# Kernel tuning notes

Hardware: AMD Instinct MI355X
Metric: run time of the kernel (lower is better)

Reference implementation:

```python
import jax, jax.numpy as jnp
import numpy as np

B, N, DIM_IN, DIM_OUT, EMBED, CHEB_K = 32, 2000, 64, 64, 16, 3


def setup_inputs() -> dict:
    key = jax.random.key(0)
    ks = jax.random.split(key, 6)
    return {
        "x": jax.random.normal(ks[0], (B, N, DIM_IN), dtype=jnp.float32),
        "node_embeddings": jax.random.normal(ks[1], (N, EMBED), dtype=jnp.float32),
        "nodevec1": jax.random.normal(ks[2], (N, EMBED), dtype=jnp.float32),
        "nodevec2": jax.random.normal(ks[3], (EMBED, N), dtype=jnp.float32),
        "weights_pool": jax.random.normal(ks[4], (EMBED, CHEB_K, DIM_IN, DIM_OUT), dtype=jnp.float32) * 0.1,
        "bias_pool": jax.random.normal(ks[5], (EMBED, DIM_OUT), dtype=jnp.float32) * 0.1,
    }


def reference(x, node_embeddings, nodevec1, nodevec2, weights_pool, bias_pool):
    n = node_embeddings.shape[0]
    # adaptive adjacency: softmax(relu(nodevec1 @ nodevec2)) over rows' neighbors
    s = jax.nn.softmax(jax.nn.relu(nodevec1 @ nodevec2), axis=1)  # [N, N]
    # Chebyshev polynomial stack: T0 = I, T1 = S, Tk = 2 S Tk-1 - Tk-2
    support_set = [jnp.eye(n, dtype=x.dtype), s]
    for _ in range(2, CHEB_K):
        support_set.append(2.0 * s @ support_set[-1] - support_set[-2])
    supports = jnp.stack(support_set, axis=0)  # [K, N, N]
    # node-conditioned weights / bias
    weights = jnp.einsum('nd,dkio->nkio', node_embeddings, weights_pool)  # [N, K, I, O]
    bias = node_embeddings @ bias_pool  # [N, O]
    # graph conv: aggregate then per-node combine
    x_g = jnp.einsum('knm,bmc->bnkc', supports, x)  # [B, N, K, I]
    out = jnp.einsum('bnki,nkio->bno', x_g, weights) + bias  # [B, N, O]
    return out
```

## Files before the change

### kernel.cpp

```cpp
#include <hip/hip_runtime.h>

#define N_NODES 2000
#define NP      2048
#define KB      63
#define KB3     66
#define BATCH   32
#define DIM     64
#define EMB     16
#define KI      192
#define WCOLS   12288

typedef __bf16 bf16;
typedef __attribute__((ext_vector_type(8))) __bf16 bf16x8;
typedef __attribute__((ext_vector_type(4))) float  f32x4;

struct alignas(8) bf16x4pk { bf16 v[4]; };

__device__ __forceinline__ void gl_lds16(const bf16* g, bf16* l) {
    __builtin_amdgcn_global_load_lds(
        (__attribute__((address_space(1))) void*)(g),
        (__attribute__((address_space(3))) void*)(l), 16, 0, 0);
}


#define Z0   (WCOLS * 32)
#define Z1   (Z0 + N_NODES * 32)
#define Z2   (Z1 + 3 * NP * 32)
#define PREP_SM_BLK   2554
#define PREP_BLOCKS   (N_NODES + 1024 + PREP_SM_BLK)

__global__ __launch_bounds__(256) void prep_fused(
    const float* __restrict__ nv1, const float* __restrict__ nv2,
    bf16* __restrict__ Sp,
    const float* __restrict__ X, bf16* __restrict__ Xtp, bf16* __restrict__ Xbf,
    const float* __restrict__ wp, const float* __restrict__ emb,
    bf16* __restrict__ wpT2, bf16* __restrict__ embp, bf16* __restrict__ Sp63)
{
    const int bid = blockIdx.x;
    const int tid = threadIdx.x;

    if (bid < N_NODES) {
        const int row = bid;
        const int j0  = tid * 8;
        __shared__ float sa[EMB];
        __shared__ float wred[4];
        __shared__ float bcast;
        if (tid < EMB) sa[tid] = nv1[row * EMB + tid];
        __syncthreads();

        const bool active = (tid < 250);
        float v[8] = {0,0,0,0,0,0,0,0};
        if (active) {
#pragma unroll
            for (int d = 0; d < EMB; ++d) {
                const float sd = sa[d];
                const float4 q0 = *(const float4*)&nv2[d * N_NODES + j0];
                const float4 q1 = *(const float4*)&nv2[d * N_NODES + j0 + 4];
                v[0] += sd * q0.x; v[1] += sd * q0.y; v[2] += sd * q0.z; v[3] += sd * q0.w;
                v[4] += sd * q1.x; v[5] += sd * q1.y; v[6] += sd * q1.z; v[7] += sd * q1.w;
            }
        }
        float lmax = 0.0f;
#pragma unroll
        for (int jj = 0; jj < 8; ++jj) { v[jj] = fmaxf(v[jj], 0.0f); lmax = fmaxf(lmax, v[jj]); }
#pragma unroll
        for (int off = 32; off > 0; off >>= 1)
            lmax = fmaxf(lmax, __shfl_down(lmax, off, 64));
        if ((tid & 63) == 0) wred[tid >> 6] = lmax;
        __syncthreads();
        if (tid == 0) bcast = fmaxf(fmaxf(wred[0], wred[1]), fmaxf(wred[2], wred[3]));
        __syncthreads();
        const float rmax = bcast;

        float lsum = 0.0f;
        if (active) {
#pragma unroll
            for (int jj = 0; jj < 8; ++jj) { v[jj] = __expf(v[jj] - rmax); lsum += v[jj]; }
        }
#pragma unroll
        for (int off = 32; off > 0; off >>= 1)
            lsum += __shfl_down(lsum, off, 64);
        if ((tid & 63) == 0) wred[tid >> 6] = lsum;
        __syncthreads();
        if (tid == 0) bcast = wred[0] + wred[1] + wred[2] + wred[3];
        __syncthreads();
        const float inv = 1.0f / bcast;

        if (tid < 252) {
            bf16x8 pk;
#pragma unroll
            for (int jj = 0; jj < 8; ++jj)
                pk[jj] = (bf16)(active ? v[jj] * inv : 0.0f);
            const int kb = j0 >> 5, q = (j0 >> 3) & 3;
            const int nt = row >> 6, r = row & 63;
            *(bf16x8*)&Sp[((size_t)(kb * 32 + nt) * 256 + q * 64 + r) * 8] = pk;
        }
    } else if (bid < N_NODES + 1024) {
        const int t  = bid - N_NODES;
        const int b  = t >> 5;
        const int m0 = (t & 31) * 64;
        __shared__ bf16 T[64][72];
#pragma unroll
        for (int i = 0; i < 4; ++i) {
            int idx = i * 256 + tid;
            int r  = idx >> 4;
            int c4 = (idx & 15) * 4;
            int m  = m0 + r;
            float4 v = make_float4(0.f, 0.f, 0.f, 0.f);
            if (m < N_NODES)
                v = *(const float4*)&X[((size_t)b * N_NODES + m) * DIM + c4];
            bf16x4pk pk;
            pk.v[0] = (bf16)v.x; pk.v[1] = (bf16)v.y;
            pk.v[2] = (bf16)v.z; pk.v[3] = (bf16)v.w;
            if (m < N_NODES)
                *(bf16x4pk*)&Xbf[((size_t)b * N_NODES + m) * DIM + c4] = pk;
            T[c4 + 0][r] = pk.v[0];
            T[c4 + 1][r] = pk.v[1];
            T[c4 + 2][r] = pk.v[2];
            T[c4 + 3][r] = pk.v[3];
        }
        __syncthreads();
#pragma unroll
        for (int i = 0; i < 2; ++i) {
            int idx = i * 256 + tid;
            int c   = idx >> 3;
            int mch = idx & 7;
            int kb  = (m0 >> 5) + (mch >> 2);
            if (kb < KB) {
                int q = mch & 3;
                bf16x8 vv = *(const bf16x8*)&T[c][mch * 8];
                *(bf16x8*)&Xtp[((size_t)(b * KB3 + kb) * 256 + q * 64 + c) * 8] = vv;
            }
        }
    } else {
        int idx = (bid - N_NODES - 1024) * 256 + tid;
        if (idx < Z0) {
            int col = idx >> 5, d = idx & 31;
            int o  = col / KI;
            int kk = col - o * KI;
            int cheb = kk >> 6, i = kk & 63;
            float v = (d < EMB) ? wp[(((d * 3 + cheb) * 64 + i) * 64) + o] : 0.0f;
            wpT2[idx] = (bf16)v;
        } else if (idx < Z1) {
            int j = idx - Z0;
            int n = j >> 5, d = j & 31;
            float v = (d < EMB) ? emb[n * EMB + d] : 0.0f;
            embp[j] = (bf16)v;
        } else if (idx < Z2) {
            Sp63[idx - Z1] = (bf16)0.0f;
        }
    }
}

__global__ __launch_bounds__(256, 2) void spmm_pack(
    const bf16* __restrict__ Ap, const bf16* __restrict__ Btp,
    bf16* __restrict__ Ybf, bf16* __restrict__ Ytp, int write_ytp)
{
    const int i = blockIdx.x;
    const int kx = i & 7, j = i >> 3;
    const int ntB = (j & 7) + 8 * (kx & 1);
    const int b   = ((j >> 3) << 2) + (kx >> 1);
    const int n0  = ntB * 128;
    const int tid = threadIdx.x;
    const int lane = tid & 63, wave = tid >> 6;
    const int l15 = lane & 15, quad = lane >> 4;

    __shared__ bf16 As[2][3 * 4096];
    __shared__ bf16 Bs[2][3 * 2048];

    const bf16* aslab = Ap  + (size_t)(ntB * 2) * 2048 + tid * 8;
    const bf16* bslab = Btp + (size_t)(b * KB3) * 2048 + tid * 8;

#define DMA_STAGE(buf, kb0_) {                                        \
        _Pragma("unroll")                                             \
        for (int jj = 0; jj < 3; ++jj) {                              \
            const bf16* pa = aslab + (size_t)(kb0_ + jj) * (32 * 2048);\
            const bf16* pb = bslab + (size_t)(kb0_ + jj) * 2048;      \
            gl_lds16(pa,        &As[buf][jj * 4096 + tid * 8]);       \
            gl_lds16(pa + 2048, &As[buf][jj * 4096 + 2048 + tid * 8]);\
            gl_lds16(pb,        &Bs[buf][jj * 2048 + tid * 8]);  } }

    f32x4 acc[2][4] = {};
    const int ga = (wave >> 1) * 256 + quad * 64 + (wave & 1) * 32;
    const int gb = quad * 64;

    DMA_STAGE(0, 0);
#pragma unroll 1
    for (int s = 0; s < 22; ++s) {
        const int cur = s & 1;
        __syncthreads();
        bf16x8 af[3][2], bfr[3][4];
#pragma unroll
        for (int jj = 0; jj < 3; ++jj) {
#pragma unroll
            for (int t = 0; t < 2; ++t)
                af[jj][t]  = *(const bf16x8*)&As[cur][jj * 4096 + (ga + t * 16 + l15) * 8];
#pragma unroll
            for (int t = 0; t < 4; ++t)
                bfr[jj][t] = *(const bf16x8*)&Bs[cur][jj * 2048 + (gb + t * 16 + l15) * 8];
        }
        if (s + 1 < 22) DMA_STAGE(cur ^ 1, (s + 1) * 3);
#pragma unroll
        for (int jj = 0; jj < 3; ++jj)
#pragma unroll
            for (int rt = 0; rt < 2; ++rt)
#pragma unroll
                for (int ct = 0; ct < 4; ++ct)
                    acc[rt][ct] = __builtin_amdgcn_mfma_f32_16x16x32_bf16(
                        af[jj][rt], bfr[jj][ct], acc[rt][ct], 0, 0, 0);
    }
#undef DMA_STAGE

#pragma unroll
    for (int rt = 0; rt < 2; ++rt) {
        const int nbase = n0 + wave * 32 + rt * 16 + quad * 4;
#pragma unroll
        for (int ct = 0; ct < 4; ++ct) {
            const int c = ct * 16 + l15;
#pragma unroll
            for (int r = 0; r < 4; ++r) {
                int n = nbase + r;
                if (n < N_NODES)
                    Ybf[((size_t)b * N_NODES + n) * DIM + c] = (bf16)acc[rt][ct][r];
            }
            if (write_ytp && nbase + 4 <= N_NODES) {
                const int kb2 = nbase >> 5;
                const int kq  = (nbase & 31) >> 3;
                const int j4  = nbase & 7;
                bf16x4pk pk;
                pk.v[0] = (bf16)acc[rt][ct][0];
                pk.v[1] = (bf16)acc[rt][ct][1];
                pk.v[2] = (bf16)acc[rt][ct][2];
                pk.v[3] = (bf16)acc[rt][ct][3];
                *(bf16x4pk*)&Ytp[((size_t)(b * KB3 + kb2) * 256 + kq * 64 + c) * 8 + j4] = pk;
            }
        }
    }
}

__global__ __launch_bounds__(256) void prep_W_mfma(
    const bf16* __restrict__ embp, const bf16* __restrict__ wpT2,
    bf16* __restrict__ W)
{
    const int colbase = blockIdx.x * 256;
    const int n0      = blockIdx.y * 16;
    const int tid  = threadIdx.x;
    const int lane = tid & 63, wave = tid >> 6;
    const int l15 = lane & 15, quad = lane >> 4;

    __shared__ bf16 Cs[16][264];

    const bf16x8 af = *(const bf16x8*)&embp[(n0 + l15) * 32 + quad * 8];
    const f32x4 zero = {};
#pragma unroll
    for (int ct = 0; ct < 4; ++ct) {
        const int col = colbase + wave * 64 + ct * 16 + l15;
        bf16x8 bfr = *(const bf16x8*)&wpT2[(size_t)col * 32 + quad * 8];
        f32x4 acc = __builtin_amdgcn_mfma_f32_16x16x32_bf16(af, bfr, zero, 0, 0, 0);
#pragma unroll
        for (int r = 0; r < 4; ++r)
            Cs[quad * 4 + r][wave * 64 + ct * 16 + l15] = (bf16)acc[r];
    }
    __syncthreads();
    {
        const int row = tid >> 4;
        const int c16 = (tid & 15) * 16;
        bf16x8 v0 = *(const bf16x8*)&Cs[row][c16];
        bf16x8 v1 = *(const bf16x8*)&Cs[row][c16 + 8];
        bf16* dst = &W[(size_t)(n0 + row) * WCOLS + colbase + c16];
        *(bf16x8*)dst       = v0;
        *(bf16x8*)(dst + 8) = v1;
    }
}

__global__ __launch_bounds__(256) void combine_node(
    const bf16* __restrict__ xbf, const bf16* __restrict__ y1bf,
    const bf16* __restrict__ y2bf, const float* __restrict__ emb,
    const float* __restrict__ bp, const bf16* __restrict__ W,
    float* __restrict__ out)
{
    const int n   = blockIdx.x;
    const int tid = threadIdx.x;
    const int lane = tid & 63, wave = tid >> 6;
    const int l15 = lane & 15, quad = lane >> 4;

    __shared__ bf16 As[BATCH][200];
    __shared__ bf16 Ws[DIM][200];
    __shared__ float bias_s[DIM];
    __shared__ float emb_s[EMB];

    if (tid < EMB) emb_s[tid] = emb[n * EMB + tid];

    {
        const int b  = tid >> 3;
        const int c8 = (tid & 7) * 8;
        const size_t base = ((size_t)b * N_NODES + n) * DIM + c8;
        bf16x8 vx = *(const bf16x8*)&xbf [base];
        bf16x8 v1 = *(const bf16x8*)&y1bf[base];
        bf16x8 v2 = *(const bf16x8*)&y2bf[base];
        bf16x8 p2;
#pragma unroll
        for (int e = 0; e < 8; ++e)
            p2[e] = (bf16)(2.0f * (float)v2[e] - (float)vx[e]);
        *(bf16x8*)&As[b][c8]       = vx;
        *(bf16x8*)&As[b][64 + c8]  = v1;
        *(bf16x8*)&As[b][128 + c8] = p2;
    }
    {
        const bf16* Wn = W + (size_t)n * WCOLS;
#pragma unroll
        for (int jj = 0; jj < 6; ++jj) {
            int chunk = jj * 256 + tid;
            int o  = chunk / 24;
            int kc = chunk - o * 24;
            bf16x8 v = *(const bf16x8*)&Wn[(size_t)chunk * 8];
            *(bf16x8*)&Ws[o][kc * 8] = v;
        }
    }
    __syncthreads();

    if (tid < DIM) {
        float s = 0.0f;
#pragma unroll
        for (int d = 0; d < EMB; ++d) s += emb_s[d] * bp[d * DIM + tid];
        bias_s[tid] = s;
    }

    bf16x8 af[2][6];
#pragma unroll
    for (int mt = 0; mt < 2; ++mt)
#pragma unroll
        for (int ks = 0; ks < 6; ++ks)
            af[mt][ks] = *(const bf16x8*)&As[mt * 16 + l15][ks * 32 + quad * 8];

    f32x4 acc[2] = {};
#pragma unroll
    for (int ks = 0; ks < 6; ++ks) {
        bf16x8 bfr = *(const bf16x8*)&Ws[wave * 16 + l15][ks * 32 + quad * 8];
        acc[0] = __builtin_amdgcn_mfma_f32_16x16x32_bf16(af[0][ks], bfr, acc[0], 0, 0, 0);
        acc[1] = __builtin_amdgcn_mfma_f32_16x16x32_bf16(af[1][ks], bfr, acc[1], 0, 0, 0);
    }
    __syncthreads();

    const int o = wave * 16 + l15;
    const float bv = bias_s[o];
#pragma unroll
    for (int mt = 0; mt < 2; ++mt)
#pragma unroll
        for (int r = 0; r < 4; ++r) {
            int b = mt * 16 + quad * 4 + r;
            out[((size_t)b * N_NODES + n) * DIM + o] = acc[mt][r] + bv;
        }
}

extern "C" void kernel_launch(void* const* d_in, const int* in_sizes, int n_in,
                              void* d_out, int out_size, void* d_ws, size_t ws_size,
                              hipStream_t stream) {
    const float* x   = (const float*)d_in[0];
    const float* emb = (const float*)d_in[1];
    const float* nv1 = (const float*)d_in[2];
    const float* nv2 = (const float*)d_in[3];
    const float* wp  = (const float*)d_in[4];
    const float* bp  = (const float*)d_in[5];
    float* out = (float*)d_out;

    char* w = (char*)d_ws;
    bf16* Sp   = (bf16*)w;  w += (size_t)KB3 * NP * 32 * 2;
    bf16* xTp  = (bf16*)w;  w += (size_t)BATCH * KB3 * DIM * 32 * 2;
    bf16* y1Tp = (bf16*)w;  w += (size_t)BATCH * KB3 * DIM * 32 * 2;
    bf16* xbf  = (bf16*)w;  w += (size_t)BATCH * N_NODES * DIM * 2;
    bf16* y1bf = (bf16*)w;  w += (size_t)BATCH * N_NODES * DIM * 2;
    bf16* y2bf = (bf16*)w;  w += (size_t)BATCH * N_NODES * DIM * 2;
    bf16* wpT2 = (bf16*)w;  w += (size_t)WCOLS * 32 * 2;
    bf16* embp = (bf16*)w;  w += (size_t)N_NODES * 32 * 2;
    bf16* W    = (bf16*)w;

    prep_fused<<<PREP_BLOCKS, 256, 0, stream>>>(
        nv1, nv2, Sp, x, xTp, xbf, wp, emb, wpT2, embp,
        Sp + (size_t)63 * NP * 32);
    prep_W_mfma<<<dim3(WCOLS / 256, N_NODES / 16), 256, 0, stream>>>(embp, wpT2, W);
    spmm_pack<<<512, 256, 0, stream>>>(Sp, xTp,  y1bf, y1Tp, 1);
    spmm_pack<<<512, 256, 0, stream>>>(Sp, y1Tp, y2bf, y1Tp, 0);
    combine_node<<<N_NODES, 256, 0, stream>>>(xbf, y1bf, y2bf, emb, bp, W, out);
}
```

Before: 167.4 us.

## Fuse weight generation into first SpMM launch and deepen K pipeline to four stages

The separate prep_W kernel is folded into the first SpMM launch as extra blocks, each covering five node groups per column tile, so W generation runs alongside the spmm blocks instead of as its own launch. The SpMM main loop moves from double-buffered 3-slab stages to a 4-deep ring of single-slab stages. It uses explicit vmcnt waits and raw barriers and raises launch bounds to 3 blocks per CU. This targets launch overhead and load latency, at the cost of 48KB LDS per block and a fragile hand-written waitcnt schedule.

```diff
diff --git a/kernel.cpp b/kernel.cpp
--- a/kernel.cpp
+++ b/kernel.cpp
@@ -28,6 +28,8 @@
 #define Z2   (Z1 + 3 * NP * 32)
 #define PREP_SM_BLK   2554
 #define PREP_BLOCKS   (N_NODES + 1024 + PREP_SM_BLK)
+
+#define PW_BLOCKS 1200
 
 __global__ __launch_bounds__(256) void prep_fused(
     const float* __restrict__ nv1, const float* __restrict__ nv2,
@@ -152,124 +154,139 @@
     }
 }
 
-__global__ __launch_bounds__(256, 2) void spmm_pack(
+__global__ __launch_bounds__(256, 3) void spmm_pipe4(
     const bf16* __restrict__ Ap, const bf16* __restrict__ Btp,
-    bf16* __restrict__ Ybf, bf16* __restrict__ Ytp, int write_ytp)
+    bf16* __restrict__ Ybf, bf16* __restrict__ Ytp,
+    const bf16* __restrict__ embp, const bf16* __restrict__ wpT2,
+    bf16* __restrict__ W, int write_ytp)
 {
-    const int i = blockIdx.x;
-    const int kx = i & 7, j = i >> 3;
-    const int ntB = (j & 7) + 8 * (kx & 1);
-    const int b   = ((j >> 3) << 2) + (kx >> 1);
-    const int n0  = ntB * 128;
-    const int tid = threadIdx.x;
+    __shared__ __align__(16) char smem[49152];
+    const int bid  = blockIdx.x;
+    const int tid  = threadIdx.x;
     const int lane = tid & 63, wave = tid >> 6;
-    const int l15 = lane & 15, quad = lane >> 4;
-
-    __shared__ bf16 As[2][3 * 4096];
-    __shared__ bf16 Bs[2][3 * 2048];
-
-    const bf16* aslab = Ap  + (size_t)(ntB * 2) * 2048 + tid * 8;
-    const bf16* bslab = Btp + (size_t)(b * KB3) * 2048 + tid * 8;
-
-#define DMA_STAGE(buf, kb0_) {                                        \
-        _Pragma("unroll")                                             \
-        for (int jj = 0; jj < 3; ++jj) {                              \
-            const bf16* pa = aslab + (size_t)(kb0_ + jj) * (32 * 2048);\
-            const bf16* pb = bslab + (size_t)(kb0_ + jj) * 2048;      \
-            gl_lds16(pa,        &As[buf][jj * 4096 + tid * 8]);       \
-            gl_lds16(pa + 2048, &As[buf][jj * 4096 + 2048 + tid * 8]);\
-            gl_lds16(pb,        &Bs[buf][jj * 2048 + tid * 8]);  } }
-
-    f32x4 acc[2][4] = {};
-    const int ga = (wave >> 1) * 256 + quad * 64 + (wave & 1) * 32;
-    const int gb = quad * 64;
-
-    DMA_STAGE(0, 0);
+    const int l15  = lane & 15, quad = lane >> 4;
+
+    if (bid < 512) {
+        bf16* As = (bf16*)smem;
+        bf16* Bs = (bf16*)(smem + 32768);
+
+        const int kx = bid & 7, j = bid >> 3;
+        const int ntB = (j & 7) + 8 * (kx & 1);
+        const int b   = ((j >> 3) << 2) + (kx >> 1);
+        const int n0  = ntB * 128;
+
+        const bf16* aslab = Ap  + (size_t)(ntB * 2) * 2048 + tid * 8;
+        const bf16* bslab = Btp + (size_t)(b * KB3) * 2048 + tid * 8;
+
+#define STAGE(buf, s_) {                                               \
+        const bf16* pa = aslab + (size_t)(s_) * (32 * 2048);           \
+        const bf16* pb = bslab + (size_t)(s_) * 2048;                  \
+        gl_lds16(pa,        &As[(buf) * 4096 + tid * 8]);              \
+        gl_lds16(pa + 2048, &As[(buf) * 4096 + 2048 + tid * 8]);       \
+        gl_lds16(pb,        &Bs[(buf) * 2048 + tid * 8]); }
+
+        f32x4 acc[2][4] = {};
+        const int ga = (wave >> 1) * 256 + quad * 64 + (wave & 1) * 32;
+        const int gb = quad * 64;
+
+        STAGE(0, 0);
+        STAGE(1, 1);
+        STAGE(2, 2);
 #pragma unroll 1
-    for (int s = 0; s < 22; ++s) {
-        const int cur = s & 1;
-        __syncthreads();
-        bf16x8 af[3][2], bfr[3][4];
-#pragma unroll
-        for (int jj = 0; jj < 3; ++jj) {
+        for (int s = 0; s < 66; ++s) {
+            const int cur = s & 3;
+            if (s < 64) {
+                asm volatile("s_waitcnt vmcnt(6)" ::: "memory");
+            } else if (s == 64) {
+                asm volatile("s_waitcnt vmcnt(3)" ::: "memory");
+            } else {
+                asm volatile("s_waitcnt vmcnt(0)" ::: "memory");
+            }
+            __builtin_amdgcn_s_barrier();
+            __builtin_amdgcn_sched_barrier(0);
+            if (s + 3 < 66) STAGE((s + 3) & 3, s + 3);
+            bf16x8 af[2], bfr[4];
 #pragma unroll
             for (int t = 0; t < 2; ++t)
-                af[jj][t]  = *(const bf16x8*)&As[cur][jj * 4096 + (ga + t * 16 + l15) * 8];
+                af[t]  = *(const bf16x8*)&As[cur * 4096 + (ga + t * 16 + l15) * 8];
 #pragma unroll
             for (int t = 0; t < 4; ++t)
-                bfr[jj][t] = *(const bf16x8*)&Bs[cur][jj * 2048 + (gb + t * 16 + l15) * 8];
-        }
-        if (s + 1 < 22) DMA_STAGE(cur ^ 1, (s + 1) * 3);
-#pragma unroll
-        for (int jj = 0; jj < 3; ++jj)
+                bfr[t] = *(const bf16x8*)&Bs[cur * 2048 + (gb + t * 16 + l15) * 8];
 #pragma unroll
             for (int rt = 0; rt < 2; ++rt)
 #pragma unroll
                 for (int ct = 0; ct < 4; ++ct)
                     acc[rt][ct] = __builtin_amdgcn_mfma_f32_16x16x32_bf16(
-                        af[jj][rt], bfr[jj][ct], acc[rt][ct], 0, 0, 0);
-    }
-#undef DMA_STAGE
-
-#pragma unroll
-    for (int rt = 0; rt < 2; ++rt) {
-        const int nbase = n0 + wave * 32 + rt * 16 + quad * 4;
+                        af[rt], bfr[ct], acc[rt][ct], 0, 0, 0);
+        }
+#undef STAGE
+
+#pragma unroll
+        for (int rt = 0; rt < 2; ++rt) {
+            const int nbase = n0 + wave * 32 + rt * 16 + quad * 4;
+#pragma unroll
+            for (int ct = 0; ct < 4; ++ct) {
+                const int c = ct * 16 + l15;
+#pragma unroll
+                for (int r = 0; r < 4; ++r) {
+                    int n = nbase + r;
+                    if (n < N_NODES)
+                        Ybf[((size_t)b * N_NODES + n) * DIM + c] = (bf16)acc[rt][ct][r];
+                }
+                if (write_ytp && nbase + 4 <= N_NODES) {
+                    const int kb2 = nbase >> 5;
+                    const int kq  = (nbase & 31) >> 3;
+                    const int j4  = nbase & 7;
+                    bf16x4pk pk;
+                    pk.v[0] = (bf16)acc[rt][ct][0];
+                    pk.v[1] = (bf16)acc[rt][ct][1];
+                    pk.v[2] = (bf16)acc[rt][ct][2];
+                    pk.v[3] = (bf16)acc[rt][ct][3];
+                    *(bf16x4pk*)&Ytp[((size_t)(b * KB3 + kb2) * 256 + kq * 64 + c) * 8 + j4] = pk;
+                }
+            }
+        }
+    } else {
+        bf16 (*Cs)[264] = (bf16(*)[264])smem;
+
+        const int pid     = bid - 512;
+        const int colbase = (pid % 48) * 256;
+        const int ng0     = (pid / 48) * 5;
+
+        bf16x8 bfr[4];
 #pragma unroll
         for (int ct = 0; ct < 4; ++ct) {
-            const int c = ct * 16 + l15;
-#pragma unroll
-            for (int r = 0; r < 4; ++r) {
-                int n = nbase + r;
-                if (n < N_NODES)
-                    Ybf[((size_t)b * N_NODES + n) * DIM + c] = (bf16)acc[rt][ct][r];
-            }
-            if (write_ytp && nbase + 4 <= N_NODES) {
-                const int kb2 = nbase >> 5;
-                const int kq  = (nbase & 31) >> 3;
-                const int j4  = nbase & 7;
-                bf16x4pk pk;
-                pk.v[0] = (bf16)acc[rt][ct][0];
-                pk.v[1] = (bf16)acc[rt][ct][1];
-                pk.v[2] = (bf16)acc[rt][ct][2];
-                pk.v[3] = (bf16)acc[rt][ct][3];
-                *(bf16x4pk*)&Ytp[((size_t)(b * KB3 + kb2) * 256 + kq * 64 + c) * 8 + j4] = pk;
-            }
-        }
-    }
-}
-
-__global__ __launch_bounds__(256) void prep_W_mfma(
-    const bf16* __restrict__ embp, const bf16* __restrict__ wpT2,
-    bf16* __restrict__ W)
-{
-    const int colbase = blockIdx.x * 256;
-    const int n0      = blockIdx.y * 16;
-    const int tid  = threadIdx.x;
-    const int lane = tid & 63, wave = tid >> 6;
-    const int l15 = lane & 15, quad = lane >> 4;
-
-    __shared__ bf16 Cs[16][264];
-
-    const bf16x8 af = *(const bf16x8*)&embp[(n0 + l15) * 32 + quad * 8];
-    const f32x4 zero = {};
-#pragma unroll
-    for (int ct = 0; ct < 4; ++ct) {
-        const int col = colbase + wave * 64 + ct * 16 + l15;
-        bf16x8 bfr = *(const bf16x8*)&wpT2[(size_t)col * 32 + quad * 8];
-        f32x4 acc = __builtin_amdgcn_mfma_f32_16x16x32_bf16(af, bfr, zero, 0, 0, 0);
-#pragma unroll
-        for (int r = 0; r < 4; ++r)
-            Cs[quad * 4 + r][wave * 64 + ct * 16 + l15] = (bf16)acc[r];
-    }
-    __syncthreads();
-    {
-        const int row = tid >> 4;
-        const int c16 = (tid & 15) * 16;
-        bf16x8 v0 = *(const bf16x8*)&Cs[row][c16];
-        bf16x8 v1 = *(const bf16x8*)&Cs[row][c16 + 8];
-        bf16* dst = &W[(size_t)(n0 + row) * WCOLS + colbase + c16];
-        *(bf16x8*)dst       = v0;
-        *(bf16x8*)(dst + 8) = v1;
+            const int col = colbase + wave * 64 + ct * 16 + l15;
+            bfr[ct] = *(const bf16x8*)&wpT2[(size_t)col * 32 + quad * 8];
+        }
+        bf16x8 afs[5];
+#pragma unroll
+        for (int g = 0; g < 5; ++g)
+            afs[g] = *(const bf16x8*)&embp[(size_t)((ng0 + g) * 16 + l15) * 32 + quad * 8];
+        const f32x4 zero = {};
+
+#pragma unroll
+        for (int g = 0; g < 5; ++g) {
+            const int n0 = (ng0 + g) * 16;
+#pragma unroll
+            for (int ct = 0; ct < 4; ++ct) {
+                f32x4 acc = __builtin_amdgcn_mfma_f32_16x16x32_bf16(afs[g], bfr[ct], zero, 0, 0, 0);
+#pragma unroll
+                for (int r = 0; r < 4; ++r)
+                    Cs[quad * 4 + r][wave * 64 + ct * 16 + l15] = (bf16)acc[r];
+            }
+            __syncthreads();
+            {
+                const int row = tid >> 4;
+                const int c16 = (tid & 15) * 16;
+                bf16x8 v0 = *(const bf16x8*)&Cs[row][c16];
+                bf16x8 v1 = *(const bf16x8*)&Cs[row][c16 + 8];
+                bf16* dst = &W[(size_t)(n0 + row) * WCOLS + colbase + c16];
+                *(bf16x8*)dst       = v0;
+                *(bf16x8*)(dst + 8) = v1;
+            }
+            __syncthreads();
+        }
     }
 }
 
@@ -378,8 +395,7 @@
     prep_fused<<<PREP_BLOCKS, 256, 0, stream>>>(
         nv1, nv2, Sp, x, xTp, xbf, wp, emb, wpT2, embp,
         Sp + (size_t)63 * NP * 32);
-    prep_W_mfma<<<dim3(WCOLS / 256, N_NODES / 16), 256, 0, stream>>>(embp, wpT2, W);
-    spmm_pack<<<512, 256, 0, stream>>>(Sp, xTp,  y1bf, y1Tp, 1);
-    spmm_pack<<<512, 256, 0, stream>>>(Sp, y1Tp, y2bf, y1Tp, 0);
+    spmm_pipe4<<<512 + PW_BLOCKS, 256, 0, stream>>>(Sp, xTp, y1bf, y1Tp, embp, wpT2, W, 1);
+    spmm_pipe4<<<512, 256, 0, stream>>>(Sp, y1Tp, y2bf, y1Tp, embp, wpT2, W, 0);
     combine_node<<<N_NODES, 256, 0, stream>>>(xbf, y1bf, y2bf, emb, bp, W, out);
 }
```

Result: no change. 165.3 us (-1.2%).
